# Performance work log

Hardware: AMD Instinct MI355X
Metric: run time of the kernel (lower is better)

The kernel has to match this reference:

```python
import jax, jax.numpy as jnp
import numpy as np

HIDDEN = 1024
NUM_HEADS = 16
HEAD_DIM = HIDDEN // NUM_HEADS
B, S = 4, 4096


def setup_inputs() -> dict:
    key = jax.random.key(0)
    ks = jax.random.split(key, 7)
    scale = 1.0 / np.sqrt(HIDDEN)
    return {
        "hidden_states": jax.random.normal(ks[0], (B, S, HIDDEN), dtype=jnp.float32),
        "Wq": jax.random.normal(ks[1], (HIDDEN, HIDDEN), dtype=jnp.float32) * scale,
        "bq": jax.random.normal(ks[2], (HIDDEN,), dtype=jnp.float32) * 0.01,
        "Wk": jax.random.normal(ks[3], (HIDDEN, HIDDEN), dtype=jnp.float32) * scale,
        "bk": jax.random.normal(ks[4], (HIDDEN,), dtype=jnp.float32) * 0.01,
        "Wv": jax.random.normal(ks[5], (HIDDEN, HIDDEN), dtype=jnp.float32) * scale,
        "bv": jax.random.normal(ks[6], (HIDDEN,), dtype=jnp.float32) * 0.01,
    }


def _split_heads(x):
    # [B, S, H*D] -> [B, H, S, D]
    b, s, _ = x.shape
    return x.reshape(b, s, NUM_HEADS, HEAD_DIM).transpose(0, 2, 1, 3)


def reference(hidden_states, Wq, bq, Wk, bk, Wv, bv):
    # Fused-style QKV: single stacked GEMM, then split + reshape to heads.
    Wqkv = jnp.concatenate([Wq, Wk, Wv], axis=1)          # [H, 3H]
    bqkv = jnp.concatenate([bq, bk, bv], axis=0)           # [3H]
    qkv = jnp.einsum("bsh,hf->bsf", hidden_states, Wqkv) + bqkv  # [B, S, 3H]
    q, k, v = jnp.split(qkv, 3, axis=-1)
    return (_split_heads(q), _split_heads(k), _split_heads(v))
```

## Files before the change

kernel.cpp:

```cpp
#include <hip/hip_runtime.h>
#include <hip/hip_bf16.h>


#define M_TOT 16384
#define N_TOT 3072
#define K_TOT 1024

typedef __bf16 bf16x8 __attribute__((ext_vector_type(8)));
typedef float f32x16 __attribute__((ext_vector_type(16)));

#define AS1(p) ((const __attribute__((address_space(1))) void*)(p))
#define AS3(p) ((__attribute__((address_space(3))) void*)(p))

__device__ __forceinline__ unsigned short f2bf(float f) {
    unsigned int u = __builtin_bit_cast(unsigned int, f);
    u += 0x7fffu + ((u >> 16) & 1u);
    return (unsigned short)(u >> 16);
}

__global__ void convert_hidden(const float* __restrict__ x,
                               unsigned short* __restrict__ y, int n4) {
    int i = blockIdx.x * blockDim.x + threadIdx.x;
    int stride = gridDim.x * blockDim.x;
    for (; i < n4; i += stride) {
        float4 v = ((const float4*)x)[i];
        ushort4 o;
        o.x = f2bf(v.x); o.y = f2bf(v.y); o.z = f2bf(v.z); o.w = f2bf(v.w);
        ((ushort4*)y)[i] = o;
    }
}

__global__ void convert_weights(const float* __restrict__ Wq,
                                const float* __restrict__ Wk,
                                const float* __restrict__ Wv,
                                unsigned short* __restrict__ Bt) {
    __shared__ unsigned short tile[64][65];
    const float* W = (blockIdx.z == 0) ? Wq : (blockIdx.z == 1) ? Wk : Wv;
    int k0 = blockIdx.y * 64;
    int f0 = blockIdx.x * 64;
    int tx = threadIdx.x & 63;
    int ty = threadIdx.x >> 6;
#pragma unroll
    for (int r = 0; r < 16; ++r) {
        int k = ty + r * 4;
        tile[k][tx] = f2bf(W[(size_t)(k0 + k) * 1024 + f0 + tx]);
    }
    __syncthreads();
#pragma unroll
    for (int r = 0; r < 16; ++r) {
        int fr = ty + r * 4;
        Bt[(size_t)(blockIdx.z * 1024 + f0 + fr) * 1024 + k0 + tx] = tile[tx][fr];
    }
}

__launch_bounds__(512, 2)
__global__ void qkv_gemm(const unsigned short* __restrict__ A,
                         const unsigned short* __restrict__ Bt,
                         const float* __restrict__ bq,
                         const float* __restrict__ bk,
                         const float* __restrict__ bv,
                         float* __restrict__ out) {
    __shared__ __align__(16) unsigned short As[4][8192];
    __shared__ __align__(16) unsigned short Bs[4][8192];

    const int tid  = threadIdx.x;
    const int wave = tid >> 6;
    const int lane = tid & 63;
    const int r5   = lane & 31;
    const int half = lane >> 5;
    const int sw2  = (r5 >> 1) & 3;

    const int xcd = blockIdx.x & 7;
    const int j   = blockIdx.x >> 3;
    const int jm  = j & 7;
    const int jn  = j >> 3;

    const int wr = wave >> 2;
    const int wc = wave & 3;

    const int tr = tid >> 2;
    const int kq = (tid & 3) ^ ((tid >> 3) & 3);
    const size_t gOff = (size_t)tr * 1024 + (size_t)kq * 8;

    int st = xcd * 3;
    int bm = (st & 7) * 8 + jm;
    int bn = (st >> 3) * 4 + jn;
    const unsigned short* gA = A  + (size_t)bm * 256 * 1024;
    const unsigned short* gB = Bt + (size_t)bn * 256 * 1024;

#define STAGE(slot, koff, bA, bB)                                               \
    do {                                                                        \
        const unsigned short* sA_ = (bA) + (size_t)(koff) + gOff;               \
        const unsigned short* sB_ = (bB) + (size_t)(koff) + gOff;               \
        unsigned short* dA_ = &As[(slot)][wave * 512];                          \
        unsigned short* dB_ = &Bs[(slot)][wave * 512];                          \
        __builtin_amdgcn_global_load_lds(AS1(sA_), AS3(dA_), 16, 0, 0);         \
        __builtin_amdgcn_global_load_lds(AS1(sA_ + 131072), AS3(dA_ + 4096),    \
                                         16, 0, 0);                             \
        __builtin_amdgcn_global_load_lds(AS1(sB_), AS3(dB_), 16, 0, 0);         \
        __builtin_amdgcn_global_load_lds(AS1(sB_ + 131072), AS3(dB_ + 4096),    \
                                         16, 0, 0);                             \
    } while (0)

#define PAIR(slotc)                                                             \
    do {                                                                        \
        const unsigned short* Au = &As[(slotc)][0];                             \
        const unsigned short* Bu = &Bs[(slotc)][0];                             \
        _Pragma("unroll") for (int ks = 0; ks < 2; ++ks) {                      \
            bf16x8 av[4], bvv[2];                                               \
            const int po = ((ks * 2 + half) ^ sw2) * 8;                         \
            _Pragma("unroll") for (int ib = 0; ib < 4; ++ib)                    \
                av[ib] = *(const bf16x8*)&Au[(wr * 128 + ib * 32 + r5) * 32 + po]; \
            _Pragma("unroll") for (int jb = 0; jb < 2; ++jb)                    \
                bvv[jb] = *(const bf16x8*)&Bu[(wc * 64 + jb * 32 + r5) * 32 + po]; \
            asm volatile("s_waitcnt lgkmcnt(0)" ::: "memory");                  \
            __builtin_amdgcn_sched_barrier(0);                                  \
            __builtin_amdgcn_s_setprio(1);                                      \
            _Pragma("unroll") for (int ib = 0; ib < 4; ++ib)                    \
                _Pragma("unroll") for (int jb = 0; jb < 2; ++jb)                \
                    acc[ib][jb] = __builtin_amdgcn_mfma_f32_32x32x16_bf16(      \
                        av[ib], bvv[jb], acc[ib][jb], 0, 0, 0);                 \
            __builtin_amdgcn_s_setprio(0);                                      \
        }                                                                       \
    } while (0)

#define UKOFF(u) ((size_t)(((u) >> 1) * 64 + ((u) & 1) * 32))

    STAGE(0, UKOFF(0), gA, gB);
    STAGE(1, UKOFF(1), gA, gB);
    STAGE(2, UKOFF(2), gA, gB);

    for (int i = 0; i < 3; ++i) {
        int bm2 = bm, bn2 = bn;
        const unsigned short *gA2 = gA, *gB2 = gB;
        if (i < 2) {
            int st2 = xcd * 3 + i + 1;
            bm2 = (st2 & 7) * 8 + jm;
            bn2 = (st2 >> 3) * 4 + jn;
            gA2 = A  + (size_t)bm2 * 256 * 1024;
            gB2 = Bt + (size_t)bn2 * 256 * 1024;
        }
        const bool lastIter = (i == 2);

        f32x16 acc[4][2] = {};

#pragma unroll 2
        for (int t = 0; t < 16; ++t) {
            if (lastIter && t == 15)
                asm volatile("s_waitcnt vmcnt(4)" ::: "memory");
            else
                asm volatile("s_waitcnt vmcnt(8)" ::: "memory");
            __builtin_amdgcn_s_barrier();
            __builtin_amdgcn_sched_barrier(0);
            {
                const int u = 2 * t + 3;
                if (u < 32)        STAGE(u & 3, UKOFF(u), gA, gB);
                else if (i < 2)    STAGE((u - 32) & 3, UKOFF(u - 32), gA2, gB2);
            }
            PAIR((2 * t) & 3);

            if (lastIter && t == 15)
                asm volatile("s_waitcnt vmcnt(0)" ::: "memory");
            else
                asm volatile("s_waitcnt vmcnt(8)" ::: "memory");
            __builtin_amdgcn_s_barrier();
            __builtin_amdgcn_sched_barrier(0);
            {
                const int u = 2 * t + 4;
                if (u < 32)        STAGE(u & 3, UKOFF(u), gA, gB);
                else if (i < 2)    STAGE((u - 32) & 3, UKOFF(u - 32), gA2, gB2);
            }
            PAIR((2 * t + 1) & 3);
        }

        {
            const int section = bn >> 2;
            const int nloc0   = (bn & 3) * 256 + wc * 64;
            const float* bias = (section == 0) ? bq : (section == 1) ? bk : bv;
            float* outsec = out + (size_t)section * (4u * 16u * 4096u * 64u);

#pragma unroll
            for (int jb = 0; jb < 2; ++jb) {
                int f = nloc0 + jb * 32 + r5;
                float bval = bias[f];
                int h = f >> 6, d = f & 63;
                size_t hb = (size_t)h * (4096u * 64u);
#pragma unroll
                for (int ib = 0; ib < 4; ++ib) {
                    int mbase = bm * 256 + wr * 128 + ib * 32 + 4 * half;
#pragma unroll
                    for (int reg = 0; reg < 16; ++reg) {
                        int m = mbase + (reg & 3) + 8 * (reg >> 2);
                        int b = m >> 12, s = m & 4095;
                        outsec[(size_t)b * (16u * 4096u * 64u) + hb + (size_t)s * 64u + d] =
                            acc[ib][jb][reg] + bval;
                    }
                }
            }
        }

        bm = bm2; bn = bn2; gA = gA2; gB = gB2;
    }
#undef STAGE
#undef PAIR
#undef UKOFF
}

extern "C" void kernel_launch(void* const* d_in, const int* in_sizes, int n_in,
                              void* d_out, int out_size, void* d_ws, size_t ws_size,
                              hipStream_t stream) {
    const float* hs = (const float*)d_in[0];
    const float* Wq = (const float*)d_in[1];
    const float* bq = (const float*)d_in[2];
    const float* Wk = (const float*)d_in[3];
    const float* bk = (const float*)d_in[4];
    const float* Wv = (const float*)d_in[5];
    const float* bv = (const float*)d_in[6];
    float* out = (float*)d_out;

    unsigned short* Abf  = (unsigned short*)d_ws;
    unsigned short* Btbf = Abf + (size_t)M_TOT * K_TOT;

    convert_hidden<<<2048, 256, 0, stream>>>(hs, Abf, (M_TOT * K_TOT) / 4);
    convert_weights<<<dim3(16, 16, 3), 256, 0, stream>>>(Wq, Wk, Wv, Btbf);
    qkv_gemm<<<256, 512, 0, stream>>>(Abf, Btbf, bq, bk, bv, out);
}
```

Baseline: 370.4 us.

## Fuse bf16 conversion kernels into GEMM via cooperative grid sync

Merges the hidden-state conversion, the weight transpose-conversion and the GEMM into one cooperative kernel. Each of the 256 blocks converts its slice of activations and three weight tiles, then a grid-wide sync precedes the GEMM. This removes two kernel launches and the gaps between them. In exchange the prologue runs at only 256 blocks with a grid barrier, and the kernel must use a cooperative launch.

Result: slower. 424.1 us (+14.5%).

```diff
diff --git a/kernel.cpp b/kernel.cpp
--- a/kernel.cpp
+++ b/kernel.cpp
@@ -1,5 +1,8 @@
 #include <hip/hip_runtime.h>
 #include <hip/hip_bf16.h>
+#include <hip/hip_cooperative_groups.h>
+
+namespace cg = cooperative_groups;
 
 
 #define M_TOT 16384
@@ -18,52 +21,65 @@
     return (unsigned short)(u >> 16);
 }
 
-__global__ void convert_hidden(const float* __restrict__ x,
-                               unsigned short* __restrict__ y, int n4) {
-    int i = blockIdx.x * blockDim.x + threadIdx.x;
-    int stride = gridDim.x * blockDim.x;
-    for (; i < n4; i += stride) {
-        float4 v = ((const float4*)x)[i];
-        ushort4 o;
-        o.x = f2bf(v.x); o.y = f2bf(v.y); o.z = f2bf(v.z); o.w = f2bf(v.w);
-        ((ushort4*)y)[i] = o;
-    }
-}
-
-__global__ void convert_weights(const float* __restrict__ Wq,
-                                const float* __restrict__ Wk,
-                                const float* __restrict__ Wv,
-                                unsigned short* __restrict__ Bt) {
-    __shared__ unsigned short tile[64][65];
-    const float* W = (blockIdx.z == 0) ? Wq : (blockIdx.z == 1) ? Wk : Wv;
-    int k0 = blockIdx.y * 64;
-    int f0 = blockIdx.x * 64;
-    int tx = threadIdx.x & 63;
-    int ty = threadIdx.x >> 6;
-#pragma unroll
-    for (int r = 0; r < 16; ++r) {
-        int k = ty + r * 4;
-        tile[k][tx] = f2bf(W[(size_t)(k0 + k) * 1024 + f0 + tx]);
-    }
-    __syncthreads();
-#pragma unroll
-    for (int r = 0; r < 16; ++r) {
-        int fr = ty + r * 4;
-        Bt[(size_t)(blockIdx.z * 1024 + f0 + fr) * 1024 + k0 + tx] = tile[tx][fr];
-    }
-}
-
 __launch_bounds__(512, 2)
-__global__ void qkv_gemm(const unsigned short* __restrict__ A,
-                         const unsigned short* __restrict__ Bt,
-                         const float* __restrict__ bq,
-                         const float* __restrict__ bk,
-                         const float* __restrict__ bv,
-                         float* __restrict__ out) {
+__global__ void qkv_fused(const float* __restrict__ hs,
+                          const float* __restrict__ Wq,
+                          const float* __restrict__ Wk,
+                          const float* __restrict__ Wv,
+                          const float* __restrict__ bq,
+                          const float* __restrict__ bk,
+                          const float* __restrict__ bv,
+                          unsigned short* __restrict__ Abf,
+                          unsigned short* __restrict__ Btbf,
+                          float* __restrict__ out) {
     __shared__ __align__(16) unsigned short As[4][8192];
     __shared__ __align__(16) unsigned short Bs[4][8192];
 
-    const int tid  = threadIdx.x;
+    const int tid = threadIdx.x;
+
+    {
+        const float4* src = (const float4*)hs + (size_t)blockIdx.x * 16384;
+        ushort4* dst = (ushort4*)Abf + (size_t)blockIdx.x * 16384;
+#pragma unroll 4
+        for (int i = tid; i < 16384; i += 512) {
+            float4 v = src[i];
+            ushort4 o;
+            o.x = f2bf(v.x); o.y = f2bf(v.y); o.z = f2bf(v.z); o.w = f2bf(v.w);
+            dst[i] = o;
+        }
+    }
+
+    {
+        unsigned short(*tile)[65] = (unsigned short(*)[65]) & As[0][0];
+        const int tx = tid & 63;
+        const int ty = tid >> 6;
+        for (int it = 0; it < 3; ++it) {
+            int g = blockIdx.x * 3 + it;
+            int z = g >> 8;
+            int rem = g & 255;
+            int k0 = (rem >> 4) * 64;
+            int f0 = (rem & 15) * 64;
+            const float* W = (z == 0) ? Wq : (z == 1) ? Wk : Wv;
+            __syncthreads();
+#pragma unroll
+            for (int r = 0; r < 8; ++r) {
+                int k = ty + r * 8;
+                tile[k][tx] = f2bf(W[(size_t)(k0 + k) * 1024 + f0 + tx]);
+            }
+            __syncthreads();
+#pragma unroll
+            for (int r = 0; r < 8; ++r) {
+                int fr = ty + r * 8;
+                Btbf[(size_t)(z * 1024 + f0 + fr) * 1024 + k0 + tx] = tile[tx][fr];
+            }
+        }
+    }
+
+    cg::this_grid().sync();
+
+    const unsigned short* __restrict__ A  = Abf;
+    const unsigned short* __restrict__ Bt = Btbf;
+
     const int wave = tid >> 6;
     const int lane = tid & 63;
     const int r5   = lane & 31;
@@ -221,7 +237,9 @@
     unsigned short* Abf  = (unsigned short*)d_ws;
     unsigned short* Btbf = Abf + (size_t)M_TOT * K_TOT;
 
-    convert_hidden<<<2048, 256, 0, stream>>>(hs, Abf, (M_TOT * K_TOT) / 4);
-    convert_weights<<<dim3(16, 16, 3), 256, 0, stream>>>(Wq, Wk, Wv, Btbf);
-    qkv_gemm<<<256, 512, 0, stream>>>(Abf, Btbf, bq, bk, bv, out);
+    void* args[] = {(void*)&hs, (void*)&Wq, (void*)&Wk, (void*)&Wv,
+                    (void*)&bq, (void*)&bk, (void*)&bv,
+                    (void*)&Abf, (void*)&Btbf, (void*)&out};
+    hipLaunchCooperativeKernel((void*)qkv_fused, dim3(256), dim3(512), args, 0,
+                               stream);
 }
```

## Simplify K-loop pipeline to one barrier per step with two-slot prefetch

Applied to the files above, without the earlier changes.

Replaces the hand-scheduled 4-slot ring with three prefetched stages, split barriers and explicit vmcnt waits. The new loop has a single __syncthreads per iteration, consumes two slots, and issues the next two stages between the LDS fragment reads and the MFMAs. It also drops the s_setprio and sched_barrier hints and leaves waitcnt placement to the compiler. The goal is fewer barriers and a simpler schedule, but __syncthreads likely drains all outstanding global loads, so the prefetch distance shrinks and memory latency may be exposed.

Result: faster. 362.9 us (-2.0%).

```diff
diff --git a/kernel.cpp b/kernel.cpp
--- a/kernel.cpp
+++ b/kernel.cpp
@@ -102,33 +102,10 @@
                                          16, 0, 0);                             \
     } while (0)
 
-#define PAIR(slotc)                                                             \
-    do {                                                                        \
-        const unsigned short* Au = &As[(slotc)][0];                             \
-        const unsigned short* Bu = &Bs[(slotc)][0];                             \
-        _Pragma("unroll") for (int ks = 0; ks < 2; ++ks) {                      \
-            bf16x8 av[4], bvv[2];                                               \
-            const int po = ((ks * 2 + half) ^ sw2) * 8;                         \
-            _Pragma("unroll") for (int ib = 0; ib < 4; ++ib)                    \
-                av[ib] = *(const bf16x8*)&Au[(wr * 128 + ib * 32 + r5) * 32 + po]; \
-            _Pragma("unroll") for (int jb = 0; jb < 2; ++jb)                    \
-                bvv[jb] = *(const bf16x8*)&Bu[(wc * 64 + jb * 32 + r5) * 32 + po]; \
-            asm volatile("s_waitcnt lgkmcnt(0)" ::: "memory");                  \
-            __builtin_amdgcn_sched_barrier(0);                                  \
-            __builtin_amdgcn_s_setprio(1);                                      \
-            _Pragma("unroll") for (int ib = 0; ib < 4; ++ib)                    \
-                _Pragma("unroll") for (int jb = 0; jb < 2; ++jb)                \
-                    acc[ib][jb] = __builtin_amdgcn_mfma_f32_32x32x16_bf16(      \
-                        av[ib], bvv[jb], acc[ib][jb], 0, 0, 0);                 \
-            __builtin_amdgcn_s_setprio(0);                                      \
-        }                                                                       \
-    } while (0)
-
 #define UKOFF(u) ((size_t)(((u) >> 1) * 64 + ((u) & 1) * 32))
 
     STAGE(0, UKOFF(0), gA, gB);
     STAGE(1, UKOFF(1), gA, gB);
-    STAGE(2, UKOFF(2), gA, gB);
 
     for (int i = 0; i < 3; ++i) {
         int bm2 = bm, bn2 = bn;
@@ -140,37 +117,40 @@
             gA2 = A  + (size_t)bm2 * 256 * 1024;
             gB2 = Bt + (size_t)bn2 * 256 * 1024;
         }
-        const bool lastIter = (i == 2);
 
         f32x16 acc[4][2] = {};
 
 #pragma unroll 2
         for (int t = 0; t < 16; ++t) {
-            if (lastIter && t == 15)
-                asm volatile("s_waitcnt vmcnt(4)" ::: "memory");
-            else
-                asm volatile("s_waitcnt vmcnt(8)" ::: "memory");
-            __builtin_amdgcn_s_barrier();
-            __builtin_amdgcn_sched_barrier(0);
-            {
-                const int u = 2 * t + 3;
-                if (u < 32)        STAGE(u & 3, UKOFF(u), gA, gB);
-                else if (i < 2)    STAGE((u - 32) & 3, UKOFF(u - 32), gA2, gB2);
+            __syncthreads();
+
+#pragma unroll
+            for (int ks = 0; ks < 4; ++ks) {
+                const int slot = (2 * t + (ks >> 1)) & 3;
+                const unsigned short* Au = &As[slot][0];
+                const unsigned short* Bu = &Bs[slot][0];
+                bf16x8 av[4], bvv[2];
+                const int po = (((ks & 1) * 2 + half) ^ sw2) * 8;
+#pragma unroll
+                for (int ib = 0; ib < 4; ++ib)
+                    av[ib] = *(const bf16x8*)&Au[(wr * 128 + ib * 32 + r5) * 32 + po];
+#pragma unroll
+                for (int jb = 0; jb < 2; ++jb)
+                    bvv[jb] = *(const bf16x8*)&Bu[(wc * 64 + jb * 32 + r5) * 32 + po];
+
+                if (ks < 2) {
+                    const int u = 2 * t + 2 + ks;
+                    if (u < 32)     STAGE(u & 3, UKOFF(u), gA, gB);
+                    else if (i < 2) STAGE((u - 32) & 3, UKOFF(u - 32), gA2, gB2);
+                }
+
+#pragma unroll
+                for (int ib = 0; ib < 4; ++ib)
+#pragma unroll
+                    for (int jb = 0; jb < 2; ++jb)
+                        acc[ib][jb] = __builtin_amdgcn_mfma_f32_32x32x16_bf16(
+                            av[ib], bvv[jb], acc[ib][jb], 0, 0, 0);
             }
-            PAIR((2 * t) & 3);
-
-            if (lastIter && t == 15)
-                asm volatile("s_waitcnt vmcnt(0)" ::: "memory");
-            else
-                asm volatile("s_waitcnt vmcnt(8)" ::: "memory");
-            __builtin_amdgcn_s_barrier();
-            __builtin_amdgcn_sched_barrier(0);
-            {
-                const int u = 2 * t + 4;
-                if (u < 32)        STAGE(u & 3, UKOFF(u), gA, gB);
-                else if (i < 2)    STAGE((u - 32) & 3, UKOFF(u - 32), gA2, gB2);
-            }
-            PAIR((2 * t + 1) & 3);
         }
 
         {
@@ -202,7 +182,6 @@
         bm = bm2; bn = bn2; gA = gA2; gB = gB2;
     }
 #undef STAGE
-#undef PAIR
 #undef UKOFF
 }
 
```
